# Performance work log

Measured on AMD Instinct MI355X. Metric: run time of the kernel, lower is better.

The kernel has to match this reference:

```python
import jax, jax.numpy as jnp
import numpy as np

B, K, D, H, L = 128, 128, 768, 8, 4
HD = D // H
FF = 4 * D
SIM = D // 4
BOOST = 0.3
SCALE = HD ** -0.5
EPS = 1e-5


def _ln(x, g, b):
    m = x.mean(-1, keepdims=True)
    v = ((x - m) ** 2).mean(-1, keepdims=True)
    return (x - m) * jax.lax.rsqrt(v + EPS) * g + b


def setup_inputs() -> dict:
    key = jax.random.key(0)
    ks = jax.random.split(key, 10)
    def n(k, shape, s=0.02):
        return jax.random.normal(k, shape, dtype=jnp.float32) * s
    return {
        'slots': jax.random.normal(ks[0], (B, K, D), dtype=jnp.float32),
        'pos_emb': n(ks[1], (1, K, D)),
        'Wq': n(ks[2], (L, D, D)),
        'Wk': n(ks[3], (L, D, D)),
        'Wv': n(ks[4], (L, D, D)),
        'Wo': n(ks[5], (L, D, D)),
        'bo': jnp.zeros((L, D), jnp.float32),
        'Wsim': n(ks[6], (L, D, SIM)),
        'g1': jnp.ones((L, D), jnp.float32),
        'b1': jnp.zeros((L, D), jnp.float32),
        'g2': jnp.ones((L, D), jnp.float32),
        'b2': jnp.zeros((L, D), jnp.float32),
        'Wff1': n(ks[7], (L, D, FF)),
        'bff1': jnp.zeros((L, FF), jnp.float32),
        'Wff2': n(ks[8], (L, FF, D)),
        'bff2': jnp.zeros((L, D), jnp.float32),
        'gf': jnp.ones((D,), jnp.float32),
        'bf': jnp.zeros((D,), jnp.float32),
    }


def reference(slots, pos_emb, Wq, Wk, Wv, Wo, bo, Wsim, g1, b1, g2, b2,
              Wff1, bff1, Wff2, bff2, gf, bf):
    x = slots + pos_emb  # K == max_slots -> full pos table
    for l in range(L):
        # --- similarity-biased multi-head self-attention (pre-norm) ---
        nx = _ln(x, g1[l], b1[l])
        q = (nx @ Wq[l]).reshape(B, K, H, HD)
        k = (nx @ Wk[l]).reshape(B, K, H, HD)
        v = (nx @ Wv[l]).reshape(B, K, H, HD)
        scores = jnp.einsum('bqhd,bkhd->bhqk', q, k) * SCALE  # [B,H,K,K]
        s = nx @ Wsim[l]  # [B,K,D/4]
        s = s / jnp.maximum(jnp.linalg.norm(s, axis=-1, keepdims=True), 1e-12)
        sim = jnp.einsum('bqc,bkc->bqk', s, s)  # cosine similarity matrix
        scores = scores + BOOST * sim[:, None, :, :]
        a = jax.nn.softmax(scores, axis=-1)
        o = jnp.einsum('bhqk,bkhd->bqhd', a, v).reshape(B, K, D)
        x = x + (o @ Wo[l] + bo[l])
        # --- feed-forward (pre-norm) ---
        nx = _ln(x, g2[l], b2[l])
        h = jax.nn.gelu(nx @ Wff1[l] + bff1[l], approximate=False)
        x = x + (h @ Wff2[l] + bff2[l])
    return _ln(x, gf, bf)
```

## Files before the change

kernel.cpp:

```cpp
#include <hip/hip_runtime.h>

typedef unsigned short u16;
typedef unsigned int u32;
typedef float f32x4 __attribute__((ext_vector_type(4)));
typedef __bf16 bf16x8 __attribute__((ext_vector_type(8)));

static constexpr int D = 768, FFD = 3072, SIMC = 192, NH = 8, HD = 96;
static constexpr int B = 128, K = 128, M = B * K, NL = 4;
static constexpr int QKVW = 2560;
static constexpr int SIMOFF = 2304;
static constexpr float QSCALE = 0.14724502f;
static constexpr float SBOOST2 = 0.6578821f;
static constexpr float EPS_F = 1e-5f;

__device__ __forceinline__ float bf2f(u16 u) {
  union { u32 i; float f; } v; v.i = ((u32)u) << 16; return v.f;
}
__device__ __forceinline__ u16 f2bf(float f) {
  union { float f; u32 i; } v; v.f = f;
  u32 u = v.i;
  u32 r = (u + 0x7FFFu + ((u >> 16) & 1u)) >> 16;
  return (u16)r;
}

__device__ __forceinline__ float fast_gelu(float x) {
  float u2 = x * (2.3020585f + 0.102944f * x * x);
  float e = __builtin_amdgcn_exp2f(u2);
  float r = __builtin_amdgcn_rcpf(1.0f + e);
  return x - x * r;
}

__device__ __forceinline__ void gload16(const void* g, void* l) {
  __builtin_amdgcn_global_load_lds(
      (const __attribute__((address_space(1))) void*)g,
      (__attribute__((address_space(3))) void*)l, 16, 0, 0);
}

__global__ __launch_bounds__(256) void addpos_kernel(
    const float* __restrict__ slots, const float* __restrict__ pos,
    u16* __restrict__ x) {
  int i = blockIdx.x * 256 + threadIdx.x;
  int m = i / D;
  int d = i - m * D;
  x[i] = f2bf(slots[i] + pos[(m & (K - 1)) * D + d]);
}

__device__ __forceinline__ float block_sum(float v, float* sbuf) {
#pragma unroll
  for (int off = 32; off > 0; off >>= 1) v += __shfl_xor(v, off, 64);
  int lane = threadIdx.x & 63, w = threadIdx.x >> 6;
  if (lane == 0) sbuf[w] = v;
  __syncthreads();
  v = sbuf[0] + sbuf[1] + sbuf[2] + sbuf[3];
  __syncthreads();
  return v;
}

template <bool OUT_BF16>
__global__ __launch_bounds__(256) void ln_kernel(
    const u16* __restrict__ x, const float* __restrict__ g,
    const float* __restrict__ b, void* __restrict__ out) {
  __shared__ float sbuf[4];
  int row = blockIdx.x, tid = threadIdx.x;
  const u16* xr = x + (size_t)row * D;
  float v0 = bf2f(xr[tid]), v1 = bf2f(xr[tid + 256]), v2 = bf2f(xr[tid + 512]);
  float s = block_sum(v0 + v1 + v2, sbuf);
  float mean = s * (1.0f / D);
  float d0 = v0 - mean, d1 = v1 - mean, d2 = v2 - mean;
  float sq = block_sum(d0 * d0 + d1 * d1 + d2 * d2, sbuf);
  float rs = rsqrtf(sq * (1.0f / D) + EPS_F);
  float y0 = d0 * rs * g[tid] + b[tid];
  float y1 = d1 * rs * g[tid + 256] + b[tid + 256];
  float y2 = d2 * rs * g[tid + 512] + b[tid + 512];
  if (OUT_BF16) {
    u16* o = (u16*)out + (size_t)row * D;
    o[tid] = f2bf(y0); o[tid + 256] = f2bf(y1); o[tid + 512] = f2bf(y2);
  } else {
    float* o = (float*)out + (size_t)row * D;
    o[tid] = y0; o[tid + 256] = y1; o[tid + 512] = y2;
  }
}

struct WAll {
  const float *wq, *wk, *wv, *wo, *wsim, *wff1, *wff2;
  u16 *tA, *tB, *tC, *tD;
};
__global__ __launch_bounds__(256) void wconv_all_kernel(WAll p, float qscale) {
  __shared__ u16 t[32][33];
  int bid = blockIdx.x;
  const float* W; u16* Wt; int N, Kd, n0, k0;
  float sc = 1.0f;
  if (bid < 2304) {
    int z = bid / 576, rem = bid - z * 576;
    W = z == 0 ? p.wq : z == 1 ? p.wk : z == 2 ? p.wv : p.wo;
    Wt = z == 0 ? p.tA : z == 1 ? p.tA + 768 * 768
       : z == 2 ? p.tA + 2 * 768 * 768 : p.tB;
    if (z == 0) sc = qscale;
    N = 768; Kd = 768;
    n0 = (rem % 24) * 32; k0 = (rem / 24) * 32;
  } else if (bid < 2448) {
    int rem = bid - 2304;
    W = p.wsim; Wt = p.tA + (size_t)SIMOFF * 768; N = SIMC; Kd = 768;
    n0 = (rem % 6) * 32; k0 = (rem / 6) * 32;
  } else if (bid < 4752) {
    int rem = bid - 2448;
    W = p.wff1; Wt = p.tC; N = FFD; Kd = 768;
    n0 = (rem % 96) * 32; k0 = (rem / 96) * 32;
  } else {
    int rem = bid - 4752;
    W = p.wff2; Wt = p.tD; N = 768; Kd = FFD;
    n0 = (rem % 24) * 32; k0 = (rem / 24) * 32;
  }
  int tid = threadIdx.x;
  int c = tid & 31, r4 = tid >> 5;
#pragma unroll
  for (int i = 0; i < 4; ++i) {
    int r = r4 + i * 8;
    t[r][c] = f2bf(W[(size_t)(k0 + r) * N + n0 + c] * sc);
  }
  __syncthreads();
#pragma unroll
  for (int i = 0; i < 4; ++i) {
    int r = r4 + i * 8;
    Wt[(size_t)(n0 + r) * Kd + k0 + c] = t[c][r];
  }
}

template <bool OUT_BF16, bool BIAS, bool GELU_, bool RESID>
__global__ __launch_bounds__(512, 2) void gemm256_kernel(
    const u16* __restrict__ A, const u16* __restrict__ Bt,
    const float* __restrict__ bias, const u16* __restrict__ resid,
    void* __restrict__ Cout, int N, int Kdim, int NBX) {
  __shared__ u16 lds[65536];
  int tid = threadIdx.x;
  int w = tid >> 6, lane = tid & 63;
  int wm = w >> 2, wn = w & 3;
  int lr = lane & 15, lg = lane >> 4;

  int nwg = gridDim.x;
  int cpx = nwg >> 3;
  int swz = (blockIdx.x & 7) * cpx + (blockIdx.x >> 3);
  int bx = swz % NBX, by = swz / NBX;
  int n0 = bx << 8, m0 = by << 8;

  int scol = ((lane & 7) ^ (lane >> 3)) << 3;
  size_t aOff = (size_t)((w << 4) + (lane >> 3)) * Kdim + scol;
  u16* ldsU = lds;

  auto stageA = [&](int buf, int h, int t) {
    const u16* g = A + (size_t)(m0 + (h << 7)) * Kdim + ((size_t)t << 6) + aOff;
    u16* l = ldsU + buf * 32768 + h * 8192 + (w << 10);
    gload16(g, l);
    gload16(g + ((size_t)Kdim << 3), l + 512);
  };
  auto stageB = [&](int buf, int h, int t) {
    const u16* g = Bt + (size_t)(n0 + (h << 7)) * Kdim + ((size_t)t << 6) + aOff;
    u16* l = ldsU + buf * 32768 + 16384 + h * 8192 + (w << 10);
    gload16(g, l);
    gload16(g + ((size_t)Kdim << 3), l + 512);
  };

  const u16* lA0p = ldsU;
  const u16* lB0p = ldsU + 16384;
  const u16* lA1p = ldsU + 32768;
  const u16* lB1p = ldsU + 49152;
  int arow = (wm * 128 + lr) * 64;
  int brow = (wn * 64 + lr) * 64;
  int swz0 = (((lg * 16)) ^ ((lr & 7) << 4)) >> 1;
  int swz1 = ((64 + lg * 16) ^ ((lr & 7) << 4)) >> 1;

  f32x4 acc[8][4] = {};
  bf16x8 ar[2][4], br[2][4];

#define READ_A_KS(BASE, MSEG, KS)                                            \
  do {                                                                       \
    _Pragma("unroll") for (int mm = 0; mm < 4; ++mm) {                       \
      const u16* p_ = (BASE) + arow + ((MSEG) * 64 + mm * 16) * 64;          \
      ar[KS][mm] = *(const bf16x8*)(p_ + ((KS) ? swz1 : swz0));              \
    }                                                                        \
  } while (0)
#define READ_B_KS(BASE, NSEG, KS)                                            \
  do {                                                                       \
    _Pragma("unroll") for (int nn = 0; nn < 2; ++nn) {                       \
      const u16* p_ = (BASE) + brow + ((NSEG) * 32 + nn * 16) * 64;          \
      br[KS][(NSEG) * 2 + nn] = *(const bf16x8*)(p_ + ((KS) ? swz1 : swz0)); \
    }                                                                        \
  } while (0)
#define MFMA_Q(MSEG, NSEG)                                                   \
  do {                                                                       \
    __builtin_amdgcn_s_setprio(1);                                           \
    _Pragma("unroll") for (int ks = 0; ks < 2; ++ks)                         \
      _Pragma("unroll") for (int mm = 0; mm < 4; ++mm)                       \
        _Pragma("unroll") for (int nn = 0; nn < 2; ++nn)                     \
          acc[(MSEG) * 4 + mm][(NSEG) * 2 + nn] =                            \
              __builtin_amdgcn_mfma_f32_16x16x32_bf16(                       \
                  ar[ks][mm], br[ks][(NSEG) * 2 + nn],                       \
                  acc[(MSEG) * 4 + mm][(NSEG) * 2 + nn], 0, 0, 0);           \
    __builtin_amdgcn_s_setprio(0);                                           \
  } while (0)
#define PSYNC()                                                              \
  do {                                                                       \
    __builtin_amdgcn_sched_barrier(0);                                       \
    asm volatile("s_waitcnt lgkmcnt(0)" ::: "memory");                       \
    __builtin_amdgcn_s_barrier();                                            \
    __builtin_amdgcn_sched_barrier(0);                                       \
  } while (0)
#define PSYNC_V(N)                                                           \
  do {                                                                       \
    __builtin_amdgcn_sched_barrier(0);                                       \
    asm volatile("s_waitcnt vmcnt(" #N ") lgkmcnt(0)" ::: "memory");         \
    __builtin_amdgcn_s_barrier();                                            \
    __builtin_amdgcn_sched_barrier(0);                                       \
  } while (0)

  int NK = Kdim >> 6, NI = NK >> 1;
  stageA(0, 0, 0); stageA(0, 1, 0); stageB(0, 0, 0); stageB(0, 1, 0);
  stageB(1, 0, 1); stageB(1, 1, 1);
  asm volatile("s_waitcnt vmcnt(4)" ::: "memory");
  __builtin_amdgcn_s_barrier();
  __builtin_amdgcn_sched_barrier(0);

  for (int i = 0; i < NI; ++i) {
    int t1 = 2 * i + 1, t2 = 2 * i + 2, t3 = 2 * i + 3;
    bool last = (i == NI - 1);
    stageA(1, 0, t1);
    READ_A_KS(lA0p, 0, 0); READ_B_KS(lB0p, 0, 0);
    READ_A_KS(lA0p, 0, 1); READ_B_KS(lB0p, 0, 1);
    MFMA_Q(0, 0);
    PSYNC();
    stageA(1, 1, t1);
    READ_B_KS(lB0p, 1, 0); READ_B_KS(lB0p, 1, 1);
    MFMA_Q(0, 1);
    PSYNC();
    if (!last) stageB(0, 0, t2);
    READ_A_KS(lA0p, 1, 0); READ_A_KS(lA0p, 1, 1);
    MFMA_Q(1, 0);
    PSYNC();
    if (!last) stageB(0, 1, t2);
    MFMA_Q(1, 1);
    if (last) PSYNC_V(0);
    else      PSYNC_V(4);
    if (!last) stageA(0, 0, t2);
    READ_A_KS(lA1p, 0, 0); READ_B_KS(lB1p, 0, 0);
    READ_A_KS(lA1p, 0, 1); READ_B_KS(lB1p, 0, 1);
    MFMA_Q(0, 0);
    PSYNC();
    if (!last) stageA(0, 1, t2);
    READ_B_KS(lB1p, 1, 0); READ_B_KS(lB1p, 1, 1);
    MFMA_Q(0, 1);
    PSYNC();
    if (!last) stageB(1, 0, t3);
    READ_A_KS(lA1p, 1, 0); READ_A_KS(lA1p, 1, 1);
    MFMA_Q(1, 0);
    PSYNC();
    if (!last) stageB(1, 1, t3);
    MFMA_Q(1, 1);
    if (last) PSYNC();
    else      PSYNC_V(4);
  }

#pragma unroll
  for (int m = 0; m < 8; ++m) {
#pragma unroll
    for (int n = 0; n < 4; ++n) {
      int col = n0 + wn * 64 + n * 16 + lr;
      float bv = BIAS ? bias[col] : 0.0f;
#pragma unroll
      for (int r = 0; r < 4; ++r) {
        int row = m0 + wm * 128 + m * 16 + lg * 4 + r;
        float v = acc[m][n][r];
        if (BIAS) v += bv;
        if (GELU_) v = fast_gelu(v);
        if (RESID) v += bf2f(resid[(size_t)row * N + col]);
        if (OUT_BF16) ((u16*)Cout)[(size_t)row * N + col] = f2bf(v);
        else ((float*)Cout)[(size_t)row * N + col] = v;
      }
    }
  }
#undef READ_A_KS
#undef READ_B_KS
#undef MFMA_Q
#undef PSYNC
#undef PSYNC_V
}

__global__ __launch_bounds__(64) void snorm_kernel(
    const u16* __restrict__ qkvb, u16* __restrict__ sbf) {
  int row = blockIdx.x, lane = threadIdx.x;
  const u16* sr = qkvb + (size_t)row * QKVW + SIMOFF;
  float v0 = bf2f(sr[lane]), v1 = bf2f(sr[lane + 64]), v2 = bf2f(sr[lane + 128]);
  float sq = v0 * v0 + v1 * v1 + v2 * v2;
#pragma unroll
  for (int off = 32; off > 0; off >>= 1) sq += __shfl_xor(sq, off, 64);
  float inv = SBOOST2 / fmaxf(sqrtf(sq), 1e-12f);
  u16* o = sbf + (size_t)row * SIMC;
  o[lane] = f2bf(v0 * inv);
  o[lane + 64] = f2bf(v1 * inv);
  o[lane + 128] = f2bf(v2 * inv);
}

__global__ __launch_bounds__(256) void attn_kernel(
    const u16* __restrict__ qkv, const u16* __restrict__ sbf,
    u16* __restrict__ ob) {
  __shared__ u16 Vt[96][136];
  __shared__ u16 Pl[4][32][136];
  int bh = blockIdx.x, b = bh >> 3, h = bh & 7;
  int tid = threadIdx.x, w = tid >> 6, lane = tid & 63;
  int lr = lane & 15, lg = lane >> 4;
  const u16* qb = qkv + (size_t)b * K * QKVW + h * HD;
  const u16* kb = qb + D;
  const u16* vb = qb + 2 * D;
  const u16* sb = sbf + (size_t)b * K * SIMC;
  for (int idx = tid; idx < 128 * 12; idx += 256) {
    int r = idx / 12, db = idx - r * 12;
    uint4 v4 = *(const uint4*)(vb + (size_t)r * QKVW + db * 8);
    u32 vv[4] = {v4.x, v4.y, v4.z, v4.w};
#pragma unroll
    for (int j = 0; j < 4; ++j) {
      Vt[db * 8 + 2 * j][r] = (u16)(vv[j] & 0xffffu);
      Vt[db * 8 + 2 * j + 1][r] = (u16)(vv[j] >> 16);
    }
  }
  int q0 = 32 * w;
  f32x4 accs[2][8] = {};
#pragma unroll
  for (int ks = 0; ks < 3; ++ks) {
    bf16x8 af[2];
#pragma unroll
    for (int m = 0; m < 2; ++m)
      af[m] = *(const bf16x8*)(qb + (size_t)(q0 + 16 * m + lr) * QKVW + ks * 32 + lg * 8);
#pragma unroll
    for (int n = 0; n < 8; ++n) {
      bf16x8 bf = *(const bf16x8*)(kb + (size_t)(16 * n + lr) * QKVW + ks * 32 + lg * 8);
#pragma unroll
      for (int m = 0; m < 2; ++m)
        accs[m][n] = __builtin_amdgcn_mfma_f32_16x16x32_bf16(af[m], bf, accs[m][n], 0, 0, 0);
    }
  }
#pragma unroll
  for (int ks = 0; ks < 6; ++ks) {
    bf16x8 af[2];
#pragma unroll
    for (int m = 0; m < 2; ++m)
      af[m] = *(const bf16x8*)(sb + (size_t)(q0 + 16 * m + lr) * SIMC + ks * 32 + lg * 8);
#pragma unroll
    for (int n = 0; n < 8; ++n) {
      bf16x8 bf = *(const bf16x8*)(sb + (size_t)(16 * n + lr) * SIMC + ks * 32 + lg * 8);
#pragma unroll
      for (int m = 0; m < 2; ++m)
        accs[m][n] = __builtin_amdgcn_mfma_f32_16x16x32_bf16(af[m], bf, accs[m][n], 0, 0, 0);
    }
  }
#pragma unroll
  for (int m = 0; m < 2; ++m) {
    float mx[4] = {-3e38f, -3e38f, -3e38f, -3e38f};
#pragma unroll
    for (int n = 0; n < 8; ++n)
#pragma unroll
      for (int r = 0; r < 4; ++r) mx[r] = fmaxf(mx[r], accs[m][n][r]);
#pragma unroll
    for (int r = 0; r < 4; ++r) {
      mx[r] = fmaxf(mx[r], __shfl_xor(mx[r], 1, 64));
      mx[r] = fmaxf(mx[r], __shfl_xor(mx[r], 2, 64));
      mx[r] = fmaxf(mx[r], __shfl_xor(mx[r], 4, 64));
      mx[r] = fmaxf(mx[r], __shfl_xor(mx[r], 8, 64));
    }
    float sm[4] = {0.f, 0.f, 0.f, 0.f};
#pragma unroll
    for (int n = 0; n < 8; ++n)
#pragma unroll
      for (int r = 0; r < 4; ++r) {
        float e = __builtin_amdgcn_exp2f(accs[m][n][r] - mx[r]);
        accs[m][n][r] = e;
        sm[r] += e;
      }
#pragma unroll
    for (int r = 0; r < 4; ++r) {
      sm[r] += __shfl_xor(sm[r], 1, 64);
      sm[r] += __shfl_xor(sm[r], 2, 64);
      sm[r] += __shfl_xor(sm[r], 4, 64);
      sm[r] += __shfl_xor(sm[r], 8, 64);
    }
    float inv[4];
#pragma unroll
    for (int r = 0; r < 4; ++r) inv[r] = 1.0f / sm[r];
#pragma unroll
    for (int n = 0; n < 8; ++n)
#pragma unroll
      for (int r = 0; r < 4; ++r)
        Pl[w][16 * m + 4 * lg + r][16 * n + lr] = f2bf(accs[m][n][r] * inv[r]);
  }
  __syncthreads();
  f32x4 acco[2][6] = {};
#pragma unroll
  for (int ks = 0; ks < 4; ++ks) {
    bf16x8 pa[2];
#pragma unroll
    for (int m = 0; m < 2; ++m)
      pa[m] = *(const bf16x8*)(&Pl[w][16 * m + lr][ks * 32 + lg * 8]);
#pragma unroll
    for (int n = 0; n < 6; ++n) {
      bf16x8 bv = *(const bf16x8*)(&Vt[16 * n + lr][ks * 32 + lg * 8]);
#pragma unroll
      for (int m = 0; m < 2; ++m)
        acco[m][n] = __builtin_amdgcn_mfma_f32_16x16x32_bf16(pa[m], bv, acco[m][n], 0, 0, 0);
    }
  }
  u16* obb = ob + (size_t)b * K * D + h * HD;
#pragma unroll
  for (int m = 0; m < 2; ++m)
#pragma unroll
    for (int n = 0; n < 6; ++n)
#pragma unroll
      for (int r = 0; r < 4; ++r)
        obb[(size_t)(q0 + 16 * m + 4 * lg + r) * D + 16 * n + lr] = f2bf(acco[m][n][r]);
}

extern "C" void kernel_launch(void* const* d_in, const int* in_sizes, int n_in,
                              void* d_out, int out_size, void* d_ws, size_t ws_size,
                              hipStream_t stream) {
  (void)in_sizes; (void)n_in; (void)out_size;
  const float* slots = (const float*)d_in[0];
  const float* pos   = (const float*)d_in[1];
  const float* Wq    = (const float*)d_in[2];
  const float* Wk    = (const float*)d_in[3];
  const float* Wv    = (const float*)d_in[4];
  const float* Wo    = (const float*)d_in[5];
  const float* bo    = (const float*)d_in[6];
  const float* Wsim  = (const float*)d_in[7];
  const float* g1    = (const float*)d_in[8];
  const float* b1    = (const float*)d_in[9];
  const float* g2    = (const float*)d_in[10];
  const float* b2    = (const float*)d_in[11];
  const float* Wff1  = (const float*)d_in[12];
  const float* bff1  = (const float*)d_in[13];
  const float* Wff2  = (const float*)d_in[14];
  const float* bff2  = (const float*)d_in[15];
  const float* gf    = (const float*)d_in[16];
  const float* bfin  = (const float*)d_in[17];

  char* p = (char*)d_ws;
  u16*   x    = (u16*)p;   p += (size_t)M * D * 2;
  u16*   nx   = (u16*)p;   p += (size_t)M * D * 2;
  u16*   qkvb = (u16*)p;   p += (size_t)M * QKVW * 2;
  u16*   ob   = (u16*)p;   p += (size_t)M * D * 2;
  u16*   sbf  = (u16*)p;   p += (size_t)M * SIMC * 2;
  u16*   wtA  = (u16*)p;   p += (size_t)QKVW * D * 2;
  u16*   wtB  = (u16*)p;   p += (size_t)D * D * 2;
  u16*   wtC  = (u16*)p;   p += (size_t)FFD * D * 2;
  u16*   wtD  = (u16*)p;   p += (size_t)D * FFD * 2;
  if ((size_t)(p - (char*)d_ws) > ws_size) return;
  u16* hb = qkvb;

  hipMemsetAsync(wtA + (size_t)(SIMOFF + SIMC) * D, 0, (size_t)64 * D * 2, stream);

  addpos_kernel<<<M * D / 256, 256, 0, stream>>>(slots, pos, x);

  int nbx_qkv = QKVW / 256, nwg_qkv = nbx_qkv * (M / 256);
  int nbx_o   = D / 256,    nwg_o   = nbx_o * (M / 256);
  int nbx_f1  = FFD / 256,  nwg_f1  = nbx_f1 * (M / 256);

  for (int l = 0; l < NL; ++l) {
    ln_kernel<true><<<M, 256, 0, stream>>>(x, g1 + l * D, b1 + l * D, nx);
    WAll wp = {Wq + (size_t)l * D * D, Wk + (size_t)l * D * D,
               Wv + (size_t)l * D * D, Wo + (size_t)l * D * D,
               Wsim + (size_t)l * D * SIMC,
               Wff1 + (size_t)l * D * FFD, Wff2 + (size_t)l * FFD * D,
               wtA, wtB, wtC, wtD};
    wconv_all_kernel<<<7056, 256, 0, stream>>>(wp, QSCALE);
    gemm256_kernel<true, false, false, false><<<nwg_qkv, 512, 0, stream>>>(
        nx, wtA, nullptr, nullptr, qkvb, QKVW, D, nbx_qkv);
    snorm_kernel<<<M, 64, 0, stream>>>(qkvb, sbf);
    attn_kernel<<<B * NH, 256, 0, stream>>>(qkvb, sbf, ob);
    gemm256_kernel<true, true, false, true><<<nwg_o, 512, 0, stream>>>(
        ob, wtB, bo + l * D, x, x, D, D, nbx_o);
    ln_kernel<true><<<M, 256, 0, stream>>>(x, g2 + l * D, b2 + l * D, nx);
    gemm256_kernel<true, true, true, false><<<nwg_f1, 512, 0, stream>>>(
        nx, wtC, bff1 + l * FFD, nullptr, hb, FFD, D, nbx_f1);
    gemm256_kernel<true, true, false, true><<<nwg_o, 512, 0, stream>>>(
        hb, wtD, bff2 + l * D, x, x, D, FFD, nbx_o);
  }
  ln_kernel<false><<<M, 256, 0, stream>>>(x, gf, bfin, d_out);
}
```

Baseline: 1.508 ms.

## Precompute per-batch cosine-similarity bias once instead of per head

The similarity matrix was recomputed by every head inside the attention kernel (6 K-steps of MFMA per head). A new simpre_kernel normalizes the sim features and computes the 128x128 similarity once per batch, stored as bf16. Attention then loads it into shared memory and uses it to initialise the score accumulators. The GEMM main loop also merges two B-stage loads and drops one sync per half-iteration. The stored bias is rounded to bf16, and the memset of the padding rows of wtA is removed.

```diff
diff --git a/kernel.cpp b/kernel.cpp
--- a/kernel.cpp
+++ b/kernel.cpp
@@ -232,12 +232,9 @@
     READ_B_KS(lB0p, 1, 0); READ_B_KS(lB0p, 1, 1);
     MFMA_Q(0, 1);
     PSYNC();
-    if (!last) stageB(0, 0, t2);
+    if (!last) { stageB(0, 0, t2); stageB(0, 1, t2); }
     READ_A_KS(lA0p, 1, 0); READ_A_KS(lA0p, 1, 1);
-    MFMA_Q(1, 0);
-    PSYNC();
-    if (!last) stageB(0, 1, t2);
-    MFMA_Q(1, 1);
+    MFMA_Q(1, 0); MFMA_Q(1, 1);
     if (last) PSYNC_V(0);
     else      PSYNC_V(4);
     if (!last) stageA(0, 0, t2);
@@ -249,12 +246,9 @@
     READ_B_KS(lB1p, 1, 0); READ_B_KS(lB1p, 1, 1);
     MFMA_Q(0, 1);
     PSYNC();
-    if (!last) stageB(1, 0, t3);
+    if (!last) { stageB(1, 0, t3); stageB(1, 1, t3); }
     READ_A_KS(lA1p, 1, 0); READ_A_KS(lA1p, 1, 1);
-    MFMA_Q(1, 0);
-    PSYNC();
-    if (!last) stageB(1, 1, t3);
-    MFMA_Q(1, 1);
+    MFMA_Q(1, 0); MFMA_Q(1, 1);
     if (last) PSYNC();
     else      PSYNC_V(4);
   }
@@ -284,23 +278,63 @@
 #undef PSYNC_V
 }
 
-__global__ __launch_bounds__(64) void snorm_kernel(
-    const u16* __restrict__ qkvb, u16* __restrict__ sbf) {
-  int row = blockIdx.x, lane = threadIdx.x;
-  const u16* sr = qkvb + (size_t)row * QKVW + SIMOFF;
-  float v0 = bf2f(sr[lane]), v1 = bf2f(sr[lane + 64]), v2 = bf2f(sr[lane + 128]);
-  float sq = v0 * v0 + v1 * v1 + v2 * v2;
-#pragma unroll
-  for (int off = 32; off > 0; off >>= 1) sq += __shfl_xor(sq, off, 64);
-  float inv = SBOOST2 / fmaxf(sqrtf(sq), 1e-12f);
-  u16* o = sbf + (size_t)row * SIMC;
-  o[lane] = f2bf(v0 * inv);
-  o[lane + 64] = f2bf(v1 * inv);
-  o[lane + 128] = f2bf(v2 * inv);
+__global__ __launch_bounds__(256) void simpre_kernel(
+    const u16* __restrict__ qkvb, u16* __restrict__ psim) {
+  __shared__ u16 sln[128][200];
+  int b = blockIdx.x, tid = threadIdx.x;
+  {
+    int row = tid >> 1, half = tid & 1;
+    const u16* sr = qkvb + ((size_t)(b * K + row)) * QKVW + SIMOFF + half * 96;
+    u16 v[96];
+    float sq = 0.f;
+#pragma unroll
+    for (int j = 0; j < 12; ++j) {
+      uint4 u4 = *(const uint4*)(sr + j * 8);
+      u32 uu[4] = {u4.x, u4.y, u4.z, u4.w};
+#pragma unroll
+      for (int t = 0; t < 4; ++t) {
+        v[j * 8 + 2 * t] = (u16)(uu[t] & 0xffffu);
+        v[j * 8 + 2 * t + 1] = (u16)(uu[t] >> 16);
+      }
+    }
+#pragma unroll
+    for (int j = 0; j < 96; ++j) { float f = bf2f(v[j]); sq += f * f; }
+    sq += __shfl_xor(sq, 1, 64);
+    float inv = SBOOST2 / fmaxf(sqrtf(sq), 1e-12f);
+#pragma unroll
+    for (int j = 0; j < 96; ++j) sln[row][half * 96 + j] = f2bf(bf2f(v[j]) * inv);
+  }
+  __syncthreads();
+  int w = tid >> 6, lane = tid & 63;
+  int lr = lane & 15, lg = lane >> 4;
+  int q0 = 32 * w;
+  f32x4 accs[2][8] = {};
+#pragma unroll
+  for (int ks = 0; ks < 6; ++ks) {
+    bf16x8 af[2];
+#pragma unroll
+    for (int m = 0; m < 2; ++m)
+      af[m] = *(const bf16x8*)(&sln[q0 + 16 * m + lr][ks * 32 + lg * 8]);
+#pragma unroll
+    for (int n = 0; n < 8; ++n) {
+      bf16x8 bf = *(const bf16x8*)(&sln[16 * n + lr][ks * 32 + lg * 8]);
+#pragma unroll
+      for (int m = 0; m < 2; ++m)
+        accs[m][n] = __builtin_amdgcn_mfma_f32_16x16x32_bf16(af[m], bf, accs[m][n], 0, 0, 0);
+    }
+  }
+  u16* pb = psim + (size_t)b * K * K;
+#pragma unroll
+  for (int m = 0; m < 2; ++m)
+#pragma unroll
+    for (int n = 0; n < 8; ++n)
+#pragma unroll
+      for (int r = 0; r < 4; ++r)
+        pb[(size_t)(q0 + 16 * m + 4 * lg + r) * K + 16 * n + lr] = f2bf(accs[m][n][r]);
 }
 
 __global__ __launch_bounds__(256) void attn_kernel(
-    const u16* __restrict__ qkv, const u16* __restrict__ sbf,
+    const u16* __restrict__ qkv, const u16* __restrict__ psim,
     u16* __restrict__ ob) {
   __shared__ u16 Vt[96][136];
   __shared__ u16 Pl[4][32][136];
@@ -310,7 +344,6 @@
   const u16* qb = qkv + (size_t)b * K * QKVW + h * HD;
   const u16* kb = qb + D;
   const u16* vb = qb + 2 * D;
-  const u16* sb = sbf + (size_t)b * K * SIMC;
   for (int idx = tid; idx < 128 * 12; idx += 256) {
     int r = idx / 12, db = idx - r * 12;
     uint4 v4 = *(const uint4*)(vb + (size_t)r * QKVW + db * 8);
@@ -321,8 +354,24 @@
       Vt[db * 8 + 2 * j + 1][r] = (u16)(vv[j] >> 16);
     }
   }
+  u16* siml = &Pl[0][0][0];
+  {
+    const u16* pb = psim + (size_t)b * K * K;
+    for (int c = tid; c < 2048; c += 256) {
+      int r = c >> 4, cc = c & 15;
+      *(uint4*)(siml + r * 136 + cc * 8) = *(const uint4*)(pb + r * 128 + cc * 8);
+    }
+  }
+  __syncthreads();
   int q0 = 32 * w;
-  f32x4 accs[2][8] = {};
+  f32x4 accs[2][8];
+#pragma unroll
+  for (int m = 0; m < 2; ++m)
+#pragma unroll
+    for (int n = 0; n < 8; ++n)
+#pragma unroll
+      for (int r = 0; r < 4; ++r)
+        accs[m][n][r] = bf2f(siml[(q0 + 16 * m + 4 * lg + r) * 136 + 16 * n + lr]);
 #pragma unroll
   for (int ks = 0; ks < 3; ++ks) {
     bf16x8 af[2];
@@ -332,20 +381,6 @@
 #pragma unroll
     for (int n = 0; n < 8; ++n) {
       bf16x8 bf = *(const bf16x8*)(kb + (size_t)(16 * n + lr) * QKVW + ks * 32 + lg * 8);
-#pragma unroll
-      for (int m = 0; m < 2; ++m)
-        accs[m][n] = __builtin_amdgcn_mfma_f32_16x16x32_bf16(af[m], bf, accs[m][n], 0, 0, 0);
-    }
-  }
-#pragma unroll
-  for (int ks = 0; ks < 6; ++ks) {
-    bf16x8 af[2];
-#pragma unroll
-    for (int m = 0; m < 2; ++m)
-      af[m] = *(const bf16x8*)(sb + (size_t)(q0 + 16 * m + lr) * SIMC + ks * 32 + lg * 8);
-#pragma unroll
-    for (int n = 0; n < 8; ++n) {
-      bf16x8 bf = *(const bf16x8*)(sb + (size_t)(16 * n + lr) * SIMC + ks * 32 + lg * 8);
 #pragma unroll
       for (int m = 0; m < 2; ++m)
         accs[m][n] = __builtin_amdgcn_mfma_f32_16x16x32_bf16(af[m], bf, accs[m][n], 0, 0, 0);
@@ -444,15 +479,13 @@
   u16*   nx   = (u16*)p;   p += (size_t)M * D * 2;
   u16*   qkvb = (u16*)p;   p += (size_t)M * QKVW * 2;
   u16*   ob   = (u16*)p;   p += (size_t)M * D * 2;
-  u16*   sbf  = (u16*)p;   p += (size_t)M * SIMC * 2;
+  u16*   psim = (u16*)p;   p += (size_t)B * K * K * 2;
   u16*   wtA  = (u16*)p;   p += (size_t)QKVW * D * 2;
   u16*   wtB  = (u16*)p;   p += (size_t)D * D * 2;
   u16*   wtC  = (u16*)p;   p += (size_t)FFD * D * 2;
   u16*   wtD  = (u16*)p;   p += (size_t)D * FFD * 2;
   if ((size_t)(p - (char*)d_ws) > ws_size) return;
   u16* hb = qkvb;
-
-  hipMemsetAsync(wtA + (size_t)(SIMOFF + SIMC) * D, 0, (size_t)64 * D * 2, stream);
 
   addpos_kernel<<<M * D / 256, 256, 0, stream>>>(slots, pos, x);
 
@@ -470,8 +503,8 @@
     wconv_all_kernel<<<7056, 256, 0, stream>>>(wp, QSCALE);
     gemm256_kernel<true, false, false, false><<<nwg_qkv, 512, 0, stream>>>(
         nx, wtA, nullptr, nullptr, qkvb, QKVW, D, nbx_qkv);
-    snorm_kernel<<<M, 64, 0, stream>>>(qkvb, sbf);
-    attn_kernel<<<B * NH, 256, 0, stream>>>(qkvb, sbf, ob);
+    simpre_kernel<<<B, 256, 0, stream>>>(qkvb, psim);
+    attn_kernel<<<B * NH, 256, 0, stream>>>(qkvb, psim, ob);
     gemm256_kernel<true, true, false, true><<<nwg_o, 512, 0, stream>>>(
         ob, wtB, bo + l * D, x, x, D, D, nbx_o);
     ln_kernel<true><<<M, 256, 0, stream>>>(x, g2 + l * D, b2 + l * D, nx);
```

After: 1.402 ms. -7.0%, faster.
